# Kernel optimization log

Measured on AMD Instinct MI355X. Metric: run time of the kernel, lower is better.

The kernel has to match this reference:

```python
import jax, jax.numpy as jnp
import numpy as np

NUM_EMBEDDINGS = 1024
EMBEDDING_DIM = 256
COMMITMENT_COST = 0.25


def setup_inputs() -> dict:
    key = jax.random.key(0)
    k1, k2 = jax.random.split(key)
    x = jax.random.normal(k1, (32, EMBEDDING_DIM, 32, 32), dtype=jnp.float32)
    codebook = jax.random.uniform(
        k2, (NUM_EMBEDDINGS, EMBEDDING_DIM), dtype=jnp.float32,
        minval=-1.0 / NUM_EMBEDDINGS, maxval=1.0 / NUM_EMBEDDINGS)
    return {"x": x, "codebook": codebook}


def reference(x, codebook):
    # x: [B, C, H, W] -> [B, H, W, C]
    inputs = jnp.transpose(x, (0, 2, 3, 1))
    B, H, W, D = inputs.shape
    K = codebook.shape[0]
    flat = inputs.reshape(-1, D)  # [N, D]

    # squared L2 distances to each code: [N, K]
    distances = (jnp.sum(flat ** 2, axis=1, keepdims=True)
                 + jnp.sum(codebook ** 2, axis=1)
                 - 2.0 * flat @ codebook.T)
    idx = jnp.argmin(distances, axis=1)  # [N]

    # gather codes (equivalent to one-hot @ codebook, without materializing one-hot)
    quantized = codebook[idx].reshape(inputs.shape)

    e_latent_loss = jnp.mean((jax.lax.stop_gradient(quantized) - inputs) ** 2)
    q_latent_loss = jnp.mean((quantized - jax.lax.stop_gradient(inputs)) ** 2)
    loss = q_latent_loss + COMMITMENT_COST * e_latent_loss

    # straight-through estimator
    quantized_st = inputs + jax.lax.stop_gradient(quantized - inputs)

    # perplexity from code usage histogram (mean of one-hot encodings)
    N = flat.shape[0]
    avg_probs = jnp.zeros((K,), dtype=flat.dtype).at[idx].add(1.0) / N
    perplexity = jnp.exp(-jnp.sum(avg_probs * jnp.log(avg_probs + 1e-10)))

    out = jnp.transpose(quantized_st, (0, 3, 1, 2))  # back to [B, C, H, W]
    return (out, loss, perplexity)
```

## Files before the change

kernel.cpp:

```cpp
#include <hip/hip_runtime.h>
#include <hip/hip_fp16.h>

typedef _Float16 half8 __attribute__((ext_vector_type(8)));
typedef _Float16 half4v __attribute__((ext_vector_type(4)));
typedef __attribute__((ext_vector_type(4))) float f32x4;

#define OUT_ELEMS 8388608


__global__ __launch_bounds__(256) void prep_kernel(const float* __restrict__ cb,
        unsigned short* __restrict__ chs, float* __restrict__ sq,
        int* __restrict__ counts, float* __restrict__ loss) {
    const int t = threadIdx.x;
    if (blockIdx.x == 0) {
        ((int4*)counts)[t] = make_int4(0, 0, 0, 0);
        if (t == 0) *loss = 0.f;
    }
    const int row = blockIdx.x * 16 + (t >> 4);
    const int d0 = (t & 15) * 16;
    const float* src = cb + row * 256 + d0;
    half8 h0, h1;
    float s = 0.f;
#pragma unroll
    for (int i = 0; i < 16; ++i) {
        const float v = src[i];
        s += v * v;
        const _Float16 h = (_Float16)(v * 1024.f);
        if (i < 8) h0[i] = h; else h1[i - 8] = h;
    }
    const int g = row >> 8, sidx = (row >> 4) & 15, m = row & 15, e = m & 7;
    const int j0 = (t & 15) * 2;
    unsigned short* tile = chs + sidx * 16384 + g * 4096 + m * 256;
    *(half8*)(tile + (((j0    ) ^ e) << 3)) = h0;
    *(half8*)(tile + (((j0 + 1) ^ e) << 3)) = h1;
#pragma unroll
    for (int off = 1; off < 16; off <<= 1) s += __shfl_xor(s, off);
    if ((t & 15) == 0) sq[row] = s;
}

__global__ __launch_bounds__(256, 2) void vq_kernel(
    const float* __restrict__ x, const float* __restrict__ cb,
    const unsigned short* __restrict__ chs, const float* __restrict__ sq,
    int* __restrict__ counts, float* __restrict__ loss_accum,
    float* __restrict__ out)
{
    __shared__ __align__(16) unsigned char Arena[65536];
    __shared__ float mv[4][64];
    __shared__ int   mk[4][64];
    __shared__ float xsqL[64];
    __shared__ int   codeL[64];

    const int t = threadIdx.x;
    const int lane = t & 63;
    const int w = t >> 6;
    const int m = lane & 15;
    const int q = lane >> 4;
    const int kb = w << 8;
    const int bid = blockIdx.x;
    const int batch = bid >> 4;
    const int hwb = (bid & 15) << 6;

    unsigned short* XL = (unsigned short*)Arena;
    {
        const float* xg = x + (size_t)batch * 262144 + hwb;
#pragma unroll
        for (int p = 0; p < 4; ++p) {
            const int id = p * 256 + t;
            const int c4 = id >> 4;
            const int hw4 = id & 15;
            const float* s0 = xg + (size_t)(c4 * 4) * 1024 + hw4 * 4;
            const f32x4 v0 = *(const f32x4*)(s0);
            const f32x4 v1 = *(const f32x4*)(s0 + 1024);
            const f32x4 v2 = *(const f32x4*)(s0 + 2048);
            const f32x4 v3 = *(const f32x4*)(s0 + 3072);
#pragma unroll
            for (int j = 0; j < 4; ++j) {
                const int hw = hw4 * 4 + j;
                const int e = (((hw & 7) ^ ((hw >> 3) & 7)) << 1);
                half4v hv;
                hv[0] = (_Float16)v0[j];
                hv[1] = (_Float16)v1[j];
                hv[2] = (_Float16)v2[j];
                hv[3] = (_Float16)v3[j];
                *(half4v*)(XL + hw * 256 + ((c4 ^ e) << 2)) = hv;
            }
        }
    }
    __syncthreads();

    const char* chsB = (const char*)chs;
    char* bsB = (char*)Arena;
    const int so = w * 8192 + lane * 16;

    {
        const char* src = chsB + so;
        char* dst = bsB + 32768 + w * 8192;
#pragma unroll
        for (int i = 0; i < 8; ++i)
            __builtin_amdgcn_global_load_lds(
                (const __attribute__((address_space(1))) void*)(src + i * 1024),
                (__attribute__((address_space(3))) void*)(dst + i * 1024), 16, 0, 0);
    }

    half8 Ah[4][8];
#pragma unroll
    for (int f = 0; f < 4; ++f) {
        const int hw = f * 16 + m;
        const unsigned short* row = XL + hw * 256;
        const int e = (((hw & 7) ^ ((hw >> 3) & 7)) << 1);
        float xs = 0.f;
#pragma unroll
        for (int ks = 0; ks < 8; ++ks) {
            const half8 a = *(const half8*)(row + (((8 * ks + 2 * q) ^ e) << 2));
            Ah[f][ks] = a;
#pragma unroll
            for (int j = 0; j < 8; ++j) { const float fv = (float)a[j]; xs = fmaf(fv, fv, xs); }
        }
        xs += __shfl_xor(xs, 16);
        xs += __shfl_xor(xs, 32);
        if (w == 0 && q == 0) xsqL[hw] = xs;
    }
    __syncthreads();

    float bestv[4][4];
    int   bestk[4][4];
#pragma unroll
    for (int f = 0; f < 4; ++f)
#pragma unroll
        for (int r = 0; r < 4; ++r) { bestv[f][r] = 3.4e38f; bestk[f][r] = 0; }

    float sc2 = sq[kb + m];

    const int rbase = w * 8192 + m * 512 + ((q ^ (m & 3)) << 4);
    const int eh = (m >> 2) & 1;

    for (int s = 0; s < 16; ++s) {
        const int buf = (s + 1) & 1;
        __syncthreads();
        if (s + 1 < 16) {
            const char* src = chsB + (s + 1) * 32768 + so;
            char* dst = bsB + (buf ^ 1) * 32768 + w * 8192;
#pragma unroll
            for (int i = 0; i < 8; ++i)
                __builtin_amdgcn_global_load_lds(
                    (const __attribute__((address_space(1))) void*)(src + i * 1024),
                    (__attribute__((address_space(3))) void*)(dst + i * 1024), 16, 0, 0);
        }
        float sc2n = 0.f;
        if (s + 1 < 16) sc2n = sq[kb + (s + 1) * 16 + m];

        f32x4 a0 = {0.f,0.f,0.f,0.f}, a1 = {0.f,0.f,0.f,0.f};
        f32x4 a2 = {0.f,0.f,0.f,0.f}, a3 = {0.f,0.f,0.f,0.f};
        const char* bp = bsB + buf * 32768 + rbase;
#pragma unroll
        for (int ks = 0; ks < 8; ++ks) {
            const half8 b = *(const half8*)(bp + ((ks ^ eh) << 6));
            a0 = __builtin_amdgcn_mfma_f32_16x16x32_f16(Ah[0][ks], b, a0, 0, 0, 0);
            a1 = __builtin_amdgcn_mfma_f32_16x16x32_f16(Ah[1][ks], b, a1, 0, 0, 0);
            a2 = __builtin_amdgcn_mfma_f32_16x16x32_f16(Ah[2][ks], b, a2, 0, 0, 0);
            a3 = __builtin_amdgcn_mfma_f32_16x16x32_f16(Ah[3][ks], b, a3, 0, 0, 0);
        }
        const int code = kb + s * 16 + m;
#pragma unroll
        for (int f = 0; f < 4; ++f) {
            const f32x4 a = (f == 0) ? a0 : (f == 1) ? a1 : (f == 2) ? a2 : a3;
#pragma unroll
            for (int r = 0; r < 4; ++r) {
                const float d0v = fmaf(-0.001953125f, a[r], sc2);
                if (d0v < bestv[f][r]) { bestv[f][r] = d0v; bestk[f][r] = code; }
            }
        }
        sc2 = sc2n;
    }

#pragma unroll
    for (int f = 0; f < 4; ++f)
#pragma unroll
        for (int r = 0; r < 4; ++r) {
            float v = bestv[f][r];
            int   k = bestk[f][r];
#pragma unroll
            for (int d = 1; d < 16; d <<= 1) {
                const float ov = __shfl_xor(v, d);
                const int   ok = __shfl_xor(k, d);
                if (ov < v || (ov == v && ok < k)) { v = ov; k = ok; }
            }
            if (m == 0) {
                const int row = f * 16 + q * 4 + r;
                mv[w][row] = v;
                mk[w][row] = k;
            }
        }
    __syncthreads();

    if (t < 64) {
        float v = mv[0][t]; int k = mk[0][t];
#pragma unroll
        for (int g2 = 1; g2 < 4; ++g2) {
            const float vg = mv[g2][t];
            const int   kg = mk[g2][t];
            if (vg < v) { v = vg; k = kg; }
        }
        codeL[t] = k;
        atomicAdd(&counts[k], 1);
        float lp = xsqL[t] + v;
#pragma unroll
        for (int off = 32; off > 0; off >>= 1) lp += __shfl_down(lp, off);
        if (t == 0) atomicAdd(loss_accum, lp);
    }
    __syncthreads();

    float* Q = (float*)Arena;
#pragma unroll
    for (int h = 0; h < 2; ++h) {
        {
            const int r = t & 31, seg = t >> 5;
            const float* src = cb + (size_t)codeL[h * 32 + r] * 256 + seg * 32;
#pragma unroll
            for (int i = 0; i < 8; ++i)
                *(f32x4*)&Q[r * 257 + seg * 32 + i * 4] = *(const f32x4*)(src + i * 4);
        }
        __syncthreads();
        {
            const int hw4 = (t & 7) * 4;
            const int c0 = t >> 3;
            float* dst = out + (size_t)batch * 262144 + hwb + h * 32 + hw4;
#pragma unroll
            for (int i = 0; i < 8; ++i) {
                const int c = c0 + i * 32;
                f32x4 v;
                v[0] = Q[(hw4 + 0) * 257 + c];
                v[1] = Q[(hw4 + 1) * 257 + c];
                v[2] = Q[(hw4 + 2) * 257 + c];
                v[3] = Q[(hw4 + 3) * 257 + c];
                *(f32x4*)(dst + (size_t)c * 1024) = v;
            }
        }
        if (h == 0) __syncthreads();
    }
}

__global__ __launch_bounds__(256) void finalize_kernel(
    const int* __restrict__ counts, const float* __restrict__ loss_accum,
    float* __restrict__ out)
{
    __shared__ float wsum[4];
    const int t = threadIdx.x;
    float s = 0.f;
#pragma unroll
    for (int mm = 0; mm < 4; ++mm) {
        const float p = (float)counts[t + 256 * mm] * (1.f / 32768.f);
        s += p * logf(p + 1e-10f);
    }
#pragma unroll
    for (int off = 32; off > 0; off >>= 1) s += __shfl_down(s, off);
    if ((t & 63) == 0) wsum[t >> 6] = s;
    __syncthreads();
    if (t == 0) {
        out[OUT_ELEMS]     = loss_accum[0] * (1.25f / 8388608.f);
        out[OUT_ELEMS + 1] = expf(-(wsum[0] + wsum[1] + wsum[2] + wsum[3]));
    }
}

extern "C" void kernel_launch(void* const* d_in, const int* in_sizes, int n_in,
                              void* d_out, int out_size, void* d_ws, size_t ws_size,
                              hipStream_t stream) {
    const float* x  = (const float*)d_in[0];
    const float* cb = (const float*)d_in[1];
    float* out = (float*)d_out;
    char* wsb = (char*)d_ws;
    int*            counts = (int*)(wsb + 0);
    float*          loss   = (float*)(wsb + 4096);
    float*          sq     = (float*)(wsb + 8192);
    unsigned short* chs    = (unsigned short*)(wsb + 16384);

    prep_kernel<<<64, 256, 0, stream>>>(cb, chs, sq, counts, loss);
    vq_kernel<<<512, 256, 0, stream>>>(x, cb, chs, sq, counts, loss, out);
    finalize_kernel<<<1, 256, 0, stream>>>(counts, loss, out);
}
```

Measured before the change: 121.9 us.

## Replace per-step block barriers with per-wave vmcnt waits in codebook pipeline

The codebook loop is restructured to drop the per-iteration __syncthreads. Each wave loads and reads only its own LDS slice, so it can instead wait on its own outstanding global-to-LDS loads with s_waitcnt vmcnt(9). The last step is peeled, the loop is unrolled by two, and the MFMA block is raised to higher issue priority with s_setprio. Input loads and output stores become nontemporal to reduce cache pollution. The scheme depends on the hand-written vmcnt count matching the exact number of outstanding loads, so later compiler or code changes could silently break it.

Result: slower. 139.1 us (+14.1%).

```diff
diff --git a/kernel.cpp b/kernel.cpp
--- a/kernel.cpp
+++ b/kernel.cpp
@@ -69,10 +69,10 @@
             const int c4 = id >> 4;
             const int hw4 = id & 15;
             const float* s0 = xg + (size_t)(c4 * 4) * 1024 + hw4 * 4;
-            const f32x4 v0 = *(const f32x4*)(s0);
-            const f32x4 v1 = *(const f32x4*)(s0 + 1024);
-            const f32x4 v2 = *(const f32x4*)(s0 + 2048);
-            const f32x4 v3 = *(const f32x4*)(s0 + 3072);
+            const f32x4 v0 = __builtin_nontemporal_load((const f32x4*)(s0));
+            const f32x4 v1 = __builtin_nontemporal_load((const f32x4*)(s0 + 1024));
+            const f32x4 v2 = __builtin_nontemporal_load((const f32x4*)(s0 + 2048));
+            const f32x4 v3 = __builtin_nontemporal_load((const f32x4*)(s0 + 3072));
 #pragma unroll
             for (int j = 0; j < 4; ++j) {
                 const int hw = hw4 * 4 + j;
@@ -101,6 +101,7 @@
                 (const __attribute__((address_space(1))) void*)(src + i * 1024),
                 (__attribute__((address_space(3))) void*)(dst + i * 1024), 16, 0, 0);
     }
+    float sc2 = sq[kb + m];
 
     half8 Ah[4][8];
 #pragma unroll
@@ -129,49 +130,58 @@
 #pragma unroll
         for (int r = 0; r < 4; ++r) { bestv[f][r] = 3.4e38f; bestk[f][r] = 0; }
 
-    float sc2 = sq[kb + m];
-
     const int rbase = w * 8192 + m * 512 + ((q ^ (m & 3)) << 4);
     const int eh = (m >> 2) & 1;
 
-    for (int s = 0; s < 16; ++s) {
-        const int buf = (s + 1) & 1;
-        __syncthreads();
-        if (s + 1 < 16) {
+#define VQ_COMPUTE(S, BUF)                                                      \
+    {                                                                           \
+        f32x4 a0 = {0.f,0.f,0.f,0.f}, a1 = {0.f,0.f,0.f,0.f};                   \
+        f32x4 a2 = {0.f,0.f,0.f,0.f}, a3 = {0.f,0.f,0.f,0.f};                   \
+        const char* bp = bsB + (BUF) * 32768 + rbase;                           \
+        __builtin_amdgcn_s_setprio(1);                                          \
+        _Pragma("unroll")                                                       \
+        for (int ks = 0; ks < 8; ++ks) {                                        \
+            const half8 b = *(const half8*)(bp + ((ks ^ eh) << 6));             \
+            a0 = __builtin_amdgcn_mfma_f32_16x16x32_f16(Ah[0][ks], b, a0,0,0,0);\
+            a1 = __builtin_amdgcn_mfma_f32_16x16x32_f16(Ah[1][ks], b, a1,0,0,0);\
+            a2 = __builtin_amdgcn_mfma_f32_16x16x32_f16(Ah[2][ks], b, a2,0,0,0);\
+            a3 = __builtin_amdgcn_mfma_f32_16x16x32_f16(Ah[3][ks], b, a3,0,0,0);\
+        }                                                                       \
+        __builtin_amdgcn_s_setprio(0);                                          \
+        const int code = kb + (S) * 16 + m;                                     \
+        _Pragma("unroll")                                                       \
+        for (int f = 0; f < 4; ++f) {                                           \
+            const f32x4 a = (f==0)?a0:(f==1)?a1:(f==2)?a2:a3;                   \
+            _Pragma("unroll")                                                   \
+            for (int r = 0; r < 4; ++r) {                                       \
+                const float d0v = fmaf(-0.001953125f, a[r], sc2);               \
+                if (d0v < bestv[f][r]) { bestv[f][r] = d0v; bestk[f][r] = code; }\
+            }                                                                   \
+        }                                                                       \
+    }
+
+#pragma unroll 2
+    for (int s = 0; s < 15; ++s) {
+        const int pbuf = s & 1;
+        {
             const char* src = chsB + (s + 1) * 32768 + so;
-            char* dst = bsB + (buf ^ 1) * 32768 + w * 8192;
+            char* dst = bsB + pbuf * 32768 + w * 8192;
 #pragma unroll
             for (int i = 0; i < 8; ++i)
                 __builtin_amdgcn_global_load_lds(
                     (const __attribute__((address_space(1))) void*)(src + i * 1024),
                     (__attribute__((address_space(3))) void*)(dst + i * 1024), 16, 0, 0);
         }
-        float sc2n = 0.f;
-        if (s + 1 < 16) sc2n = sq[kb + (s + 1) * 16 + m];
-
-        f32x4 a0 = {0.f,0.f,0.f,0.f}, a1 = {0.f,0.f,0.f,0.f};
-        f32x4 a2 = {0.f,0.f,0.f,0.f}, a3 = {0.f,0.f,0.f,0.f};
-        const char* bp = bsB + buf * 32768 + rbase;
-#pragma unroll
-        for (int ks = 0; ks < 8; ++ks) {
-            const half8 b = *(const half8*)(bp + ((ks ^ eh) << 6));
-            a0 = __builtin_amdgcn_mfma_f32_16x16x32_f16(Ah[0][ks], b, a0, 0, 0, 0);
-            a1 = __builtin_amdgcn_mfma_f32_16x16x32_f16(Ah[1][ks], b, a1, 0, 0, 0);
-            a2 = __builtin_amdgcn_mfma_f32_16x16x32_f16(Ah[2][ks], b, a2, 0, 0, 0);
-            a3 = __builtin_amdgcn_mfma_f32_16x16x32_f16(Ah[3][ks], b, a3, 0, 0, 0);
-        }
-        const int code = kb + s * 16 + m;
-#pragma unroll
-        for (int f = 0; f < 4; ++f) {
-            const f32x4 a = (f == 0) ? a0 : (f == 1) ? a1 : (f == 2) ? a2 : a3;
-#pragma unroll
-            for (int r = 0; r < 4; ++r) {
-                const float d0v = fmaf(-0.001953125f, a[r], sc2);
-                if (d0v < bestv[f][r]) { bestv[f][r] = d0v; bestk[f][r] = code; }
-            }
-        }
-        sc2 = sc2n;
-    }
+        const float sq_next = sq[kb + (s + 1) * 16 + m];
+        asm volatile("s_waitcnt vmcnt(9)" ::: "memory");
+        __builtin_amdgcn_sched_barrier(0);
+        VQ_COMPUTE(s, pbuf ^ 1)
+        sc2 = sq_next;
+    }
+    asm volatile("s_waitcnt vmcnt(0)" ::: "memory");
+    __builtin_amdgcn_sched_barrier(0);
+    VQ_COMPUTE(15, 0)
+#undef VQ_COMPUTE
 
 #pragma unroll
     for (int f = 0; f < 4; ++f)
@@ -233,7 +243,7 @@
                 v[1] = Q[(hw4 + 1) * 257 + c];
                 v[2] = Q[(hw4 + 2) * 257 + c];
                 v[3] = Q[(hw4 + 3) * 257 + c];
-                *(f32x4*)(dst + (size_t)c * 1024) = v;
+                __builtin_nontemporal_store(v, (f32x4*)(dst + (size_t)c * 1024));
             }
         }
         if (h == 0) __syncthreads();
```

## Double codebook tile reuse with 512-thread blocks and register-staged prefetch

Applied to the files above, without the earlier changes.

Each block now covers 128 spatial positions with 8 waves instead of 64 with 4, so every codebook tile staged in shared memory feeds twice as many rows and total codebook traffic is halved. The async global-to-LDS loads are replaced by register prefetch of the next tile, written to LDS with an XOR swizzle after the MFMAs, and prep now stores the fp16 codebook in plain row-major order. The block count halves to 256, which may reduce occupancy and latency hiding, and the register staging adds VGPR pressure.

New measurement: 124.8 us. 1.02x slower.

```diff
diff --git a/kernel.cpp b/kernel.cpp
--- a/kernel.cpp
+++ b/kernel.cpp
@@ -28,46 +28,57 @@
         const _Float16 h = (_Float16)(v * 1024.f);
         if (i < 8) h0[i] = h; else h1[i - 8] = h;
     }
-    const int g = row >> 8, sidx = (row >> 4) & 15, m = row & 15, e = m & 7;
-    const int j0 = (t & 15) * 2;
-    unsigned short* tile = chs + sidx * 16384 + g * 4096 + m * 256;
-    *(half8*)(tile + (((j0    ) ^ e) << 3)) = h0;
-    *(half8*)(tile + (((j0 + 1) ^ e) << 3)) = h1;
+    *(half8*)(chs + row * 256 + d0)     = h0;
+    *(half8*)(chs + row * 256 + d0 + 8) = h1;
 #pragma unroll
     for (int off = 1; off < 16; off <<= 1) s += __shfl_xor(s, off);
     if ((t & 15) == 0) sq[row] = s;
 }
 
-__global__ __launch_bounds__(256, 2) void vq_kernel(
+__global__ __launch_bounds__(512, 2) void vq_kernel(
     const float* __restrict__ x, const float* __restrict__ cb,
     const unsigned short* __restrict__ chs, const float* __restrict__ sq,
     int* __restrict__ counts, float* __restrict__ loss_accum,
     float* __restrict__ out)
 {
     __shared__ __align__(16) unsigned char Arena[65536];
-    __shared__ float mv[4][64];
-    __shared__ int   mk[4][64];
-    __shared__ float xsqL[64];
-    __shared__ int   codeL[64];
+    __shared__ float mv[4][128];
+    __shared__ int   mk[4][128];
+    __shared__ float xsqL[128];
+    __shared__ int   codeL[128];
+    __shared__ float wsum[2];
 
     const int t = threadIdx.x;
     const int lane = t & 63;
-    const int w = t >> 6;
+    const int w  = t >> 6;
+    const int wg = w >> 1;
+    const int wl = w & 1;
     const int m = lane & 15;
     const int q = lane >> 4;
-    const int kb = w << 8;
+    const int kb = wg << 8;
+    const int rowb = wl << 6;
     const int bid = blockIdx.x;
-    const int batch = bid >> 4;
-    const int hwb = (bid & 15) << 6;
+    const int batch = bid >> 3;
+    const int hwb = (bid & 7) << 7;
+
+    const int cs = t >> 3, sg = cs >> 4, sm = cs & 15;
+    const int sj0 = (t & 7) * 4;
+    const unsigned short* srow = chs + ((sg << 8) + sm) * 256 + sj0 * 8;
+    half8 n0, n1, n2, n3;
+    n0 = *(const half8*)(srow);
+    n1 = *(const half8*)(srow + 8);
+    n2 = *(const half8*)(srow + 16);
+    n3 = *(const half8*)(srow + 24);
+    float sc2 = sq[kb + m];
 
     unsigned short* XL = (unsigned short*)Arena;
     {
         const float* xg = x + (size_t)batch * 262144 + hwb;
 #pragma unroll
         for (int p = 0; p < 4; ++p) {
-            const int id = p * 256 + t;
-            const int c4 = id >> 4;
-            const int hw4 = id & 15;
+            const int id = p * 512 + t;
+            const int c4 = id >> 5;
+            const int hw4 = id & 31;
             const float* s0 = xg + (size_t)(c4 * 4) * 1024 + hw4 * 4;
             const f32x4 v0 = *(const f32x4*)(s0);
             const f32x4 v1 = *(const f32x4*)(s0 + 1024);
@@ -88,24 +99,10 @@
     }
     __syncthreads();
 
-    const char* chsB = (const char*)chs;
-    char* bsB = (char*)Arena;
-    const int so = w * 8192 + lane * 16;
-
-    {
-        const char* src = chsB + so;
-        char* dst = bsB + 32768 + w * 8192;
-#pragma unroll
-        for (int i = 0; i < 8; ++i)
-            __builtin_amdgcn_global_load_lds(
-                (const __attribute__((address_space(1))) void*)(src + i * 1024),
-                (__attribute__((address_space(3))) void*)(dst + i * 1024), 16, 0, 0);
-    }
-
     half8 Ah[4][8];
 #pragma unroll
     for (int f = 0; f < 4; ++f) {
-        const int hw = f * 16 + m;
+        const int hw = rowb + f * 16 + m;
         const unsigned short* row = XL + hw * 256;
         const int e = (((hw & 7) ^ ((hw >> 3) & 7)) << 1);
         float xs = 0.f;
@@ -118,9 +115,18 @@
         }
         xs += __shfl_xor(xs, 16);
         xs += __shfl_xor(xs, 32);
-        if (w == 0 && q == 0) xsqL[hw] = xs;
-    }
-    __syncthreads();
+        if (wg == 0 && q == 0) xsqL[hw] = xs;
+    }
+    __syncthreads();
+
+    unsigned short* Bs = (unsigned short*)Arena;
+    {
+        unsigned short* wb = Bs + cs * 256;
+        *(half8*)(wb + (((sj0 + 0) ^ (sm & 7)) << 3)) = n0;
+        *(half8*)(wb + (((sj0 + 1) ^ (sm & 7)) << 3)) = n1;
+        *(half8*)(wb + (((sj0 + 2) ^ (sm & 7)) << 3)) = n2;
+        *(half8*)(wb + (((sj0 + 3) ^ (sm & 7)) << 3)) = n3;
+    }
 
     float bestv[4][4];
     int   bestk[4][4];
@@ -129,32 +135,27 @@
 #pragma unroll
         for (int r = 0; r < 4; ++r) { bestv[f][r] = 3.4e38f; bestk[f][r] = 0; }
 
-    float sc2 = sq[kb + m];
-
-    const int rbase = w * 8192 + m * 512 + ((q ^ (m & 3)) << 4);
-    const int eh = (m >> 2) & 1;
+    const unsigned short* brow = Bs + (wg * 16 + m) * 256;
+    const int eswz = m & 7;
 
     for (int s = 0; s < 16; ++s) {
-        const int buf = (s + 1) & 1;
+        const int buf = s & 1;
+        float sqn = 0.f;
+        if (s + 1 < 16) {
+            const unsigned short* sp = srow + (s + 1) * 4096;
+            n0 = *(const half8*)(sp);
+            n1 = *(const half8*)(sp + 8);
+            n2 = *(const half8*)(sp + 16);
+            n3 = *(const half8*)(sp + 24);
+            sqn = sq[kb + (s + 1) * 16 + m];
+        }
         __syncthreads();
-        if (s + 1 < 16) {
-            const char* src = chsB + (s + 1) * 32768 + so;
-            char* dst = bsB + (buf ^ 1) * 32768 + w * 8192;
-#pragma unroll
-            for (int i = 0; i < 8; ++i)
-                __builtin_amdgcn_global_load_lds(
-                    (const __attribute__((address_space(1))) void*)(src + i * 1024),
-                    (__attribute__((address_space(3))) void*)(dst + i * 1024), 16, 0, 0);
-        }
-        float sc2n = 0.f;
-        if (s + 1 < 16) sc2n = sq[kb + (s + 1) * 16 + m];
-
         f32x4 a0 = {0.f,0.f,0.f,0.f}, a1 = {0.f,0.f,0.f,0.f};
         f32x4 a2 = {0.f,0.f,0.f,0.f}, a3 = {0.f,0.f,0.f,0.f};
-        const char* bp = bsB + buf * 32768 + rbase;
+        const unsigned short* bp = brow + buf * 16384;
 #pragma unroll
         for (int ks = 0; ks < 8; ++ks) {
-            const half8 b = *(const half8*)(bp + ((ks ^ eh) << 6));
+            const half8 b = *(const half8*)(bp + (((ks * 4 + q) ^ eswz) << 3));
             a0 = __builtin_amdgcn_mfma_f32_16x16x32_f16(Ah[0][ks], b, a0, 0, 0, 0);
             a1 = __builtin_amdgcn_mfma_f32_16x16x32_f16(Ah[1][ks], b, a1, 0, 0, 0);
             a2 = __builtin_amdgcn_mfma_f32_16x16x32_f16(Ah[2][ks], b, a2, 0, 0, 0);
@@ -170,7 +171,14 @@
                 if (d0v < bestv[f][r]) { bestv[f][r] = d0v; bestk[f][r] = code; }
             }
         }
-        sc2 = sc2n;
+        if (s + 1 < 16) {
+            unsigned short* wb = Bs + (buf ^ 1) * 16384 + cs * 256;
+            *(half8*)(wb + (((sj0 + 0) ^ (sm & 7)) << 3)) = n0;
+            *(half8*)(wb + (((sj0 + 1) ^ (sm & 7)) << 3)) = n1;
+            *(half8*)(wb + (((sj0 + 2) ^ (sm & 7)) << 3)) = n2;
+            *(half8*)(wb + (((sj0 + 3) ^ (sm & 7)) << 3)) = n3;
+            sc2 = sqn;
+        }
     }
 
 #pragma unroll
@@ -186,14 +194,14 @@
                 if (ov < v || (ov == v && ok < k)) { v = ov; k = ok; }
             }
             if (m == 0) {
-                const int row = f * 16 + q * 4 + r;
-                mv[w][row] = v;
-                mk[w][row] = k;
-            }
-        }
-    __syncthreads();
-
-    if (t < 64) {
+                const int row = rowb + f * 16 + q * 4 + r;
+                mv[wg][row] = v;
+                mk[wg][row] = k;
+            }
+        }
+    __syncthreads();
+
+    if (t < 128) {
         float v = mv[0][t]; int k = mk[0][t];
 #pragma unroll
         for (int g2 = 1; g2 < 4; ++g2) {
@@ -206,19 +214,20 @@
         float lp = xsqL[t] + v;
 #pragma unroll
         for (int off = 32; off > 0; off >>= 1) lp += __shfl_down(lp, off);
-        if (t == 0) atomicAdd(loss_accum, lp);
-    }
-    __syncthreads();
+        if ((t & 63) == 0) wsum[t >> 6] = lp;
+    }
+    __syncthreads();
+    if (t == 0) atomicAdd(loss_accum, wsum[0] + wsum[1]);
 
     float* Q = (float*)Arena;
 #pragma unroll
-    for (int h = 0; h < 2; ++h) {
+    for (int h = 0; h < 4; ++h) {
         {
             const int r = t & 31, seg = t >> 5;
-            const float* src = cb + (size_t)codeL[h * 32 + r] * 256 + seg * 32;
-#pragma unroll
-            for (int i = 0; i < 8; ++i)
-                *(f32x4*)&Q[r * 257 + seg * 32 + i * 4] = *(const f32x4*)(src + i * 4);
+            const float* src = cb + (size_t)codeL[h * 32 + r] * 256 + seg * 16;
+#pragma unroll
+            for (int i = 0; i < 4; ++i)
+                *(f32x4*)&Q[r * 257 + seg * 16 + i * 4] = *(const f32x4*)(src + i * 4);
         }
         __syncthreads();
         {
@@ -226,8 +235,8 @@
             const int c0 = t >> 3;
             float* dst = out + (size_t)batch * 262144 + hwb + h * 32 + hw4;
 #pragma unroll
-            for (int i = 0; i < 8; ++i) {
-                const int c = c0 + i * 32;
+            for (int i = 0; i < 4; ++i) {
+                const int c = c0 + i * 64;
                 f32x4 v;
                 v[0] = Q[(hw4 + 0) * 257 + c];
                 v[1] = Q[(hw4 + 1) * 257 + c];
@@ -236,7 +245,7 @@
                 *(f32x4*)(dst + (size_t)c * 1024) = v;
             }
         }
-        if (h == 0) __syncthreads();
+        if (h < 3) __syncthreads();
     }
 }
 
@@ -275,6 +284,6 @@
     unsigned short* chs    = (unsigned short*)(wsb + 16384);
 
     prep_kernel<<<64, 256, 0, stream>>>(cb, chs, sq, counts, loss);
-    vq_kernel<<<512, 256, 0, stream>>>(x, cb, chs, sq, counts, loss, out);
+    vq_kernel<<<256, 512, 0, stream>>>(x, cb, chs, sq, counts, loss, out);
     finalize_kernel<<<1, 256, 0, stream>>>(counts, loss, out);
 }
```
